# Kernel tuning notes

Hardware: AMD Instinct MI355X
Metric: run time of the kernel (lower is better)

## Reference

```python
import jax, jax.numpy as jnp
import numpy as np

N_NODES = 100000
N_EDGES = 3200000
IN_CH, HID, OUT_CH = 512, 16, 64


def gcn_conv(x, src, dst, W, b, n_nodes):
    """GCNConv: x @ W, then sym-normalized aggregation with self-loops."""
    xw = x @ W  # [N, F_out]
    loop = jnp.arange(n_nodes, dtype=src.dtype)
    s = jnp.concatenate([src, loop])  # sources (messages gathered here)
    d = jnp.concatenate([dst, loop])  # targets (messages scattered here)
    deg = jax.ops.segment_sum(jnp.ones_like(d, dtype=xw.dtype), d, num_segments=n_nodes)
    dinv = jnp.where(deg > 0, jax.lax.rsqrt(deg), 0.0)
    norm = dinv[s] * dinv[d]  # [E+N]
    msgs = xw[s] * norm[:, None]  # gather + scale
    out = jax.ops.segment_sum(msgs, d, num_segments=n_nodes)
    return out + b


def setup_inputs() -> dict:
    key = jax.random.key(0)
    k1, k2, k3, k4, k5 = jax.random.split(key, 5)
    x = jax.random.normal(k1, (N_NODES, IN_CH), dtype=jnp.float32)
    edge_index = jax.random.randint(k2, (2, N_EDGES), 0, N_NODES, dtype=jnp.int32)
    # Glorot-style init for GCNConv linear weights, zero bias (PyG default)
    W1 = jax.random.normal(k3, (IN_CH, HID), dtype=jnp.float32) * (1.0 / np.sqrt(IN_CH))
    b1 = jnp.zeros((HID,), dtype=jnp.float32)
    W2 = jax.random.normal(k4, (HID, OUT_CH), dtype=jnp.float32) * (1.0 / np.sqrt(HID))
    b2 = jnp.zeros((OUT_CH,), dtype=jnp.float32)
    return {"x": x, "edge_index": edge_index, "W1": W1, "b1": b1, "W2": W2, "b2": b2}


def reference(x, edge_index, W1, b1, W2, b2):
    # eval mode: dropout(p=0.5) is identity
    src, dst = edge_index[0], edge_index[1]
    h = gcn_conv(x, src, dst, W1, b1, N_NODES)
    h = jax.nn.relu(h)
    out = gcn_conv(h, src, dst, W2, b2, N_NODES)
    return out
```

## Files before the change

kernel.cpp:

```cpp
#include <hip/hip_runtime.h>

#define N_NODES 100000
#define N_EDGES 3200000
#define IN_CH 512
#define HID 16
#define OUT_CH 64

#define NB1 98
#define CAP1 34816
#define LEAF 64
#define CAP2 2560
#define NLEAF 1563
#define NLEAF_SLOTS (NB1 * 16)
#define BIN1_CHUNK 4096
#define BIN1_BLOCKS ((N_EDGES + BIN1_CHUNK - 1) / BIN1_CHUNK)
#define BIN2_SPLIT 9
#define BIN2_CHUNK 3872

typedef float f4 __attribute__((ext_vector_type(4)));
typedef unsigned int v2u __attribute__((ext_vector_type(2)));
typedef unsigned int v4u __attribute__((ext_vector_type(4)));

__device__ __forceinline__ unsigned rne(float f) {
    unsigned u = __float_as_uint(f);
    return (u + 0x7fffu + ((u >> 16) & 1u)) >> 16;
}
__device__ __forceinline__ v2u pk4(f4 f) {
    v2u r;
    r.x = rne(f.x) | (rne(f.y) << 16);
    r.y = rne(f.z) | (rne(f.w) << 16);
    return r;
}
__device__ __forceinline__ f4 up_lo(v4u v) {
    f4 r;
    r.x = __uint_as_float(v.x << 16);
    r.y = __uint_as_float(v.x & 0xffff0000u);
    r.z = __uint_as_float(v.y << 16);
    r.w = __uint_as_float(v.y & 0xffff0000u);
    return r;
}
__device__ __forceinline__ f4 up_hi(v4u v) {
    f4 r;
    r.x = __uint_as_float(v.z << 16);
    r.y = __uint_as_float(v.z & 0xffff0000u);
    r.z = __uint_as_float(v.w << 16);
    r.w = __uint_as_float(v.w & 0xffff0000u);
    return r;
}
__device__ __forceinline__ v4u pk8(f4 lo, f4 hi) {
    v4u r;
    r.x = rne(lo.x) | (rne(lo.y) << 16);
    r.y = rne(lo.z) | (rne(lo.w) << 16);
    r.z = rne(hi.x) | (rne(hi.y) << 16);
    r.w = rne(hi.z) | (rne(hi.w) << 16);
    return r;
}


__global__ void k_init_bcur(int* bcur1, int* bcur2, int* off) {
    int i = blockIdx.x * blockDim.x + threadIdx.x;
    if (i < NB1) bcur1[i] = i * CAP1;
    if (i < NLEAF_SLOTS) bcur2[i] = i * CAP2;
    if (i == 0) off[N_NODES] = N_EDGES;
}


__global__ __launch_bounds__(256) void k_bin1(const int* __restrict__ src,
                                              const int* __restrict__ dst,
                                              int* __restrict__ pairs1,
                                              int* __restrict__ bcur1) {
    __shared__ int cnt[NB1];
    __shared__ int base[NB1];
    const int tid = threadIdx.x;
    const int lo = blockIdx.x * BIN1_CHUNK;
    const int hi = min(lo + BIN1_CHUNK, N_EDGES);
    if (tid < NB1) cnt[tid] = 0;
    __syncthreads();
    for (int i = lo + tid; i < hi; i += 256) {
        int d = __builtin_nontemporal_load(dst + i);
        atomicAdd(&cnt[d >> 10], 1);
    }
    __syncthreads();
    if (tid < NB1 && cnt[tid] > 0) base[tid] = atomicAdd(&bcur1[tid], cnt[tid]);
    __syncthreads();
    if (tid < NB1) cnt[tid] = 0;
    __syncthreads();
    for (int i = lo + tid; i < hi; i += 256) {
        int d = __builtin_nontemporal_load(dst + i);
        int s = __builtin_nontemporal_load(src + i);
        int b = d >> 10;
        int r = atomicAdd(&cnt[b], 1);
        pairs1[base[b] + r] = (s << 10) | (d & 1023);
    }
}


__global__ __launch_bounds__(256) void k_bin2(const int* __restrict__ pairs1,
                                              const int* __restrict__ bcur1,
                                              int* __restrict__ pairs2,
                                              int* __restrict__ bcur2) {
    __shared__ int cnt[16];
    __shared__ int base[16];
    const int b = blockIdx.x / BIN2_SPLIT;
    const int s = blockIdx.x % BIN2_SPLIT;
    const int tid = threadIdx.x;
    const int len = bcur1[b] - b * CAP1;
    const int lo = b * CAP1 + min(s * BIN2_CHUNK, len);
    const int hi = b * CAP1 + min((s + 1) * BIN2_CHUNK, len);
    if (tid < 16) cnt[tid] = 0;
    __syncthreads();
    for (int i = lo + tid; i < hi; i += 256)
        atomicAdd(&cnt[(pairs1[i] & 1023) >> 6], 1);
    __syncthreads();
    if (tid < 16 && cnt[tid] > 0) base[tid] = atomicAdd(&bcur2[b * 16 + tid], cnt[tid]);
    __syncthreads();
    if (tid < 16) cnt[tid] = 0;
    __syncthreads();
    for (int i = lo + tid; i < hi; i += 256) {
        int e = pairs1[i];
        int l = (e & 1023) >> 6;
        int r = atomicAdd(&cnt[l], 1);
        pairs2[base[l] + r] = e;
    }
}


__global__ __launch_bounds__(256) void k_leafscan(const int* __restrict__ bcur2,
                                                  int* __restrict__ leafoff) {
    __shared__ int sm[256];
    __shared__ int carry;
    const int tid = threadIdx.x;
    if (tid == 0) carry = 0;
    __syncthreads();
    for (int r = 0; r < (NLEAF_SLOTS + 255) / 256; ++r) {
        int idx = r * 256 + tid;
        int v = (idx < NLEAF_SLOTS) ? (bcur2[idx] - idx * CAP2) : 0;
        sm[tid] = v;
        __syncthreads();
        for (int st = 1; st < 256; st <<= 1) {
            int t = (tid >= st) ? sm[tid - st] : 0;
            __syncthreads();
            sm[tid] += t;
            __syncthreads();
        }
        if (idx < NLEAF_SLOTS) leafoff[idx] = carry + sm[tid] - v;
        int tot = sm[255];
        __syncthreads();
        if (tid == 0) carry += tot;
        __syncthreads();
    }
}


__global__ __launch_bounds__(256) void k_scatter2(const int* __restrict__ pairs2,
                                                  const int* __restrict__ bcur2,
                                                  const int* __restrict__ leafoff,
                                                  int* __restrict__ off,
                                                  float* __restrict__ dinv,
                                                  int* __restrict__ csr) {
    __shared__ int cnt[LEAF];
    __shared__ int lcur[LEAF];
    __shared__ int buf[CAP2];
    const int leaf = blockIdx.x;
    const int tid = threadIdx.x;
    const int base2 = leaf * CAP2;
    const int len = min(bcur2[leaf] - base2, CAP2);
    const int obase = leafoff[leaf];
    if (tid < LEAF) cnt[tid] = 0;
    __syncthreads();
    for (int i = tid; i < len; i += 256)
        atomicAdd(&cnt[pairs2[base2 + i] & 63], 1);
    __syncthreads();
    if (tid < LEAF) {
        int v = cnt[tid];
        int s = v;
        for (int d = 1; d < LEAF; d <<= 1) {
            int t = __shfl_up(s, d, 64);
            if (tid >= d) s += t;
        }
        int excl = s - v;
        lcur[tid] = excl;
        int node = leaf * LEAF + tid;
        if (node < N_NODES) {
            off[node] = obase + excl;
            dinv[node] = rsqrtf((float)(1 + v));
        }
    }
    __syncthreads();
    for (int i = tid; i < len; i += 256) {
        int e = pairs2[base2 + i];
        int p = atomicAdd(&lcur[e & 63], 1);
        buf[p] = e >> 10;
    }
    __syncthreads();
    for (int i = tid; i < len; i += 256)
        csr[obase + i] = buf[i];
}


#define G1_BS 256
#define G1_NODES 128
#define G1_KT 64
#define G1_STRIDE (G1_KT + 4)

__global__ __launch_bounds__(G1_BS) void k_gemm1(const float* __restrict__ x,
                                                 const float* __restrict__ W1,
                                                 const float* __restrict__ dinv,
                                                 unsigned short* __restrict__ y1) {
    __shared__ float xt[G1_NODES * G1_STRIDE];
    __shared__ float wt[G1_KT * HID];
    const int tid = threadIdx.x;
    const int nl = tid >> 2;
    const int cg = tid & 3;
    const int node_base = blockIdx.x * G1_NODES;

    f4 acc0 = {0.f, 0.f, 0.f, 0.f};
    f4 acc1 = {0.f, 0.f, 0.f, 0.f};

    for (int kt = 0; kt < IN_CH; kt += G1_KT) {
        __syncthreads();
        for (int j = 0; j < 8; ++j) {
            int f = j * G1_BS + tid;
            int r = f >> 4;
            int c4 = f & 15;
            int gr = node_base + r;
            f4 v = {0.f, 0.f, 0.f, 0.f};
            if (gr < N_NODES)
                v = *(const f4*)(x + (size_t)gr * IN_CH + kt + c4 * 4);
            *(f4*)(xt + r * G1_STRIDE + c4 * 4) = v;
        }
        {
            int r = tid >> 2;
            int c4 = tid & 3;
            *(f4*)(wt + r * HID + c4 * 4) =
                *(const f4*)(W1 + (size_t)(kt + r) * HID + c4 * 4);
        }
        __syncthreads();

        for (int kk = 0; kk < G1_KT; kk += 4) {
            f4 x0 = *(const f4*)(xt + nl * G1_STRIDE + kk);
            f4 x1 = *(const f4*)(xt + (nl + 64) * G1_STRIDE + kk);
            f4 w0 = *(const f4*)(wt + (kk + 0) * HID + cg * 4);
            f4 w1 = *(const f4*)(wt + (kk + 1) * HID + cg * 4);
            f4 w2 = *(const f4*)(wt + (kk + 2) * HID + cg * 4);
            f4 w3 = *(const f4*)(wt + (kk + 3) * HID + cg * 4);
            acc0 += x0.x * w0; acc0 += x0.y * w1;
            acc0 += x0.z * w2; acc0 += x0.w * w3;
            acc1 += x1.x * w0; acc1 += x1.y * w1;
            acc1 += x1.z * w2; acc1 += x1.w * w3;
        }
    }

    int n0 = node_base + nl;
    int n1 = n0 + 64;
    if (n0 < N_NODES) {
        float dv = dinv[n0];
        __builtin_nontemporal_store(pk4(acc0 * dv),
            (v2u*)(y1 + (size_t)n0 * HID + cg * 4));
    }
    if (n1 < N_NODES) {
        float dv = dinv[n1];
        __builtin_nontemporal_store(pk4(acc1 * dv),
            (v2u*)(y1 + (size_t)n1 * HID + cg * 4));
    }
}


__global__ __launch_bounds__(256) void k_layer1(const unsigned short* __restrict__ y1,
                                                const int* __restrict__ off,
                                                const int* __restrict__ csr,
                                                const float* __restrict__ b1,
                                                unsigned short* __restrict__ y2) {
    int t = blockIdx.x * blockDim.x + threadIdx.x;
    int n = t >> 1;
    int hf = (t & 1) * 8;
    if (n >= N_NODES) return;
    int base = off[n];
    int cnt = off[n + 1] - base;
    f4 l0 = {0,0,0,0}, h0 = {0,0,0,0}, l1 = {0,0,0,0}, h1 = {0,0,0,0};
    f4 l2 = {0,0,0,0}, h2 = {0,0,0,0}, l3 = {0,0,0,0}, h3 = {0,0,0,0};
    int p = 0;
    for (; p + 4 <= cnt; p += 4) {
        int s0 = csr[base + p + 0];
        int s1 = csr[base + p + 1];
        int s2 = csr[base + p + 2];
        int s3 = csr[base + p + 3];
        v4u g0 = *(const v4u*)(y1 + (size_t)s0 * HID + hf);
        v4u g1 = *(const v4u*)(y1 + (size_t)s1 * HID + hf);
        v4u g2 = *(const v4u*)(y1 + (size_t)s2 * HID + hf);
        v4u g3 = *(const v4u*)(y1 + (size_t)s3 * HID + hf);
        l0 += up_lo(g0); h0 += up_hi(g0);
        l1 += up_lo(g1); h1 += up_hi(g1);
        l2 += up_lo(g2); h2 += up_hi(g2);
        l3 += up_lo(g3); h3 += up_hi(g3);
    }
    for (; p < cnt; ++p) {
        v4u g = *(const v4u*)(y1 + (size_t)csr[base + p] * HID + hf);
        l0 += up_lo(g); h0 += up_hi(g);
    }
    f4 alo = (l0 + l1) + (l2 + l3);
    f4 ahi = (h0 + h1) + (h2 + h3);
    float dv = rsqrtf((float)(cnt + 1));
    v4u gs = *(const v4u*)(y1 + (size_t)n * HID + hf);
    alo += up_lo(gs);
    ahi += up_hi(gs);
    f4 blo = ((const f4*)b1)[(t & 1) * 2 + 0];
    f4 bhi = ((const f4*)b1)[(t & 1) * 2 + 1];
    f4 rlo, rhi;
    rlo.x = fmaxf(dv * alo.x + blo.x, 0.f) * dv;
    rlo.y = fmaxf(dv * alo.y + blo.y, 0.f) * dv;
    rlo.z = fmaxf(dv * alo.z + blo.z, 0.f) * dv;
    rlo.w = fmaxf(dv * alo.w + blo.w, 0.f) * dv;
    rhi.x = fmaxf(dv * ahi.x + bhi.x, 0.f) * dv;
    rhi.y = fmaxf(dv * ahi.y + bhi.y, 0.f) * dv;
    rhi.z = fmaxf(dv * ahi.z + bhi.z, 0.f) * dv;
    rhi.w = fmaxf(dv * ahi.w + bhi.w, 0.f) * dv;
    __builtin_nontemporal_store(pk8(rlo, rhi), (v4u*)(y2 + (size_t)n * HID + hf));
}


__global__ __launch_bounds__(256) void k_layer2(const unsigned short* __restrict__ y2,
                                                const int* __restrict__ off,
                                                const int* __restrict__ csr,
                                                const float* __restrict__ W2,
                                                const float* __restrict__ b2,
                                                float* __restrict__ out) {
    __shared__ float w2[HID * OUT_CH];
    __shared__ float bs[OUT_CH];
    int tid = threadIdx.x;
    for (int j = tid; j < HID * OUT_CH; j += 256) w2[j] = W2[j];
    if (tid < OUT_CH) bs[tid] = b2[tid];
    __syncthreads();

    int t = blockIdx.x * blockDim.x + tid;
    int n = t >> 1;
    int cg = t & 1;
    int hf = cg * 8;
    if (n >= N_NODES) return;
    int base = off[n];
    int cnt = off[n + 1] - base;
    f4 l0 = {0,0,0,0}, h0 = {0,0,0,0}, l1 = {0,0,0,0}, h1 = {0,0,0,0};
    f4 l2 = {0,0,0,0}, h2 = {0,0,0,0}, l3 = {0,0,0,0}, h3 = {0,0,0,0};
    int p = 0;
    for (; p + 4 <= cnt; p += 4) {
        int s0 = csr[base + p + 0];
        int s1 = csr[base + p + 1];
        int s2 = csr[base + p + 2];
        int s3 = csr[base + p + 3];
        v4u g0 = *(const v4u*)(y2 + (size_t)s0 * HID + hf);
        v4u g1 = *(const v4u*)(y2 + (size_t)s1 * HID + hf);
        v4u g2 = *(const v4u*)(y2 + (size_t)s2 * HID + hf);
        v4u g3 = *(const v4u*)(y2 + (size_t)s3 * HID + hf);
        l0 += up_lo(g0); h0 += up_hi(g0);
        l1 += up_lo(g1); h1 += up_hi(g1);
        l2 += up_lo(g2); h2 += up_hi(g2);
        l3 += up_lo(g3); h3 += up_hi(g3);
    }
    for (; p < cnt; ++p) {
        v4u g = *(const v4u*)(y2 + (size_t)csr[base + p] * HID + hf);
        l0 += up_lo(g); h0 += up_hi(g);
    }
    f4 alo = (l0 + l1) + (l2 + l3);
    f4 ahi = (h0 + h1) + (h2 + h3);
    float dv = rsqrtf((float)(cnt + 1));
    v4u gs = *(const v4u*)(y2 + (size_t)n * HID + hf);
    alo += up_lo(gs);
    ahi += up_hi(gs);
    float zown[8] = {dv * alo.x, dv * alo.y, dv * alo.z, dv * alo.w,
                     dv * ahi.x, dv * ahi.y, dv * ahi.z, dv * ahi.w};
    float z[16];
#pragma unroll
    for (int j = 0; j < 8; ++j) {
        float zp = __shfl_xor(zown[j], 1, 64);
        z[hf + j] = zown[j];
        z[(8 - hf) + j] = zp;
    }
    f4 o[8];
#pragma unroll
    for (int j = 0; j < 8; ++j) o[j] = ((const f4*)bs)[j * 2 + cg];
#pragma unroll
    for (int cc = 0; cc < HID; ++cc) {
        const float* wr = w2 + cc * OUT_CH;
        float zz = z[cc];
#pragma unroll
        for (int j = 0; j < 8; ++j)
            o[j] += zz * *(const f4*)(wr + (j * 2 + cg) * 4);
    }
    float* orow = out + (size_t)n * OUT_CH;
#pragma unroll
    for (int j = 0; j < 8; ++j)
        __builtin_nontemporal_store(o[j], (f4*)(orow + (j * 2 + cg) * 4));
}


extern "C" void kernel_launch(void* const* d_in, const int* in_sizes, int n_in,
                              void* d_out, int out_size, void* d_ws, size_t ws_size,
                              hipStream_t stream) {
    const float* x  = (const float*)d_in[0];
    const int*   ei = (const int*)d_in[1];
    const float* W1 = (const float*)d_in[2];
    const float* b1 = (const float*)d_in[3];
    const float* W2 = (const float*)d_in[4];
    const float* b2 = (const float*)d_in[5];
    float* out = (float*)d_out;

    const int* src = ei;
    const int* dst = ei + N_EDGES;

    char* w = (char*)d_ws;
    const size_t SN = 409600;
    float* dinv     = (float*)(w);
    int*   off      = (int*)(w + SN);
    int*   bcur1    = (int*)(w + 2 * SN);
    int*   bcur2    = (int*)(w + 2 * SN + 8192);
    int*   leafoff  = (int*)(w + 2 * SN + 16384);
    char*  regB     = w + 3 * SN;
    int*   pairs1   = (int*)regB;
    int*   csr      = (int*)regB;
    char*  regC     = regB + (size_t)NB1 * CAP1 * 4;
    int*   pairs2   = (int*)regC;
    unsigned short* y1 = (unsigned short*)regC;
    unsigned short* y2 = (unsigned short*)(regC + 3200000);

    k_init_bcur<<<(NLEAF_SLOTS + 255) / 256, 256, 0, stream>>>(bcur1, bcur2, off);
    k_bin1<<<BIN1_BLOCKS, 256, 0, stream>>>(src, dst, pairs1, bcur1);
    k_bin2<<<NB1 * BIN2_SPLIT, 256, 0, stream>>>(pairs1, bcur1, pairs2, bcur2);
    k_leafscan<<<1, 256, 0, stream>>>(bcur2, leafoff);
    k_scatter2<<<NLEAF, 256, 0, stream>>>(pairs2, bcur2, leafoff, off, dinv, csr);
    k_gemm1<<<(N_NODES + G1_NODES - 1) / G1_NODES, G1_BS, 0, stream>>>(x, W1, dinv, y1);
    k_layer1<<<(N_NODES * 2 + 255) / 256, 256, 0, stream>>>(y1, off, csr, b1, y2);
    k_layer2<<<(N_NODES * 2 + 255) / 256, 256, 0, stream>>>(y2, off, csr, W2, b2, out);
}
```

Before: 214.2 us.

## Replace two-level edge binning with single-pass 256-node buckets and block-local CSR scatter

Result: slower. 224.6 us (+4.8%).

```diff
diff --git a/kernel.cpp b/kernel.cpp
--- a/kernel.cpp
+++ b/kernel.cpp
@@ -6,16 +6,10 @@
 #define HID 16
 #define OUT_CH 64
 
-#define NB1 98
-#define CAP1 34816
-#define LEAF 64
-#define CAP2 2560
-#define NLEAF 1563
-#define NLEAF_SLOTS (NB1 * 16)
+#define NB 391
+#define BCAP 9472
 #define BIN1_CHUNK 4096
 #define BIN1_BLOCKS ((N_EDGES + BIN1_CHUNK - 1) / BIN1_CHUNK)
-#define BIN2_SPLIT 9
-#define BIN2_CHUNK 3872
 
 typedef float f4 __attribute__((ext_vector_type(4)));
 typedef unsigned int v2u __attribute__((ext_vector_type(2)));
@@ -57,10 +51,9 @@
 }
 
 
-__global__ void k_init_bcur(int* bcur1, int* bcur2, int* off) {
+__global__ void k_init(int* bcur1, int* off) {
     int i = blockIdx.x * blockDim.x + threadIdx.x;
-    if (i < NB1) bcur1[i] = i * CAP1;
-    if (i < NLEAF_SLOTS) bcur2[i] = i * CAP2;
+    if (i < NB) bcur1[i] = i * BCAP;
     if (i == 0) off[N_NODES] = N_EDGES;
 }
 
@@ -69,132 +62,95 @@
                                               const int* __restrict__ dst,
                                               int* __restrict__ pairs1,
                                               int* __restrict__ bcur1) {
-    __shared__ int cnt[NB1];
-    __shared__ int base[NB1];
+    __shared__ int cnt[NB];
+    __shared__ int base[NB];
     const int tid = threadIdx.x;
     const int lo = blockIdx.x * BIN1_CHUNK;
     const int hi = min(lo + BIN1_CHUNK, N_EDGES);
-    if (tid < NB1) cnt[tid] = 0;
+    for (int j = tid; j < NB; j += 256) cnt[j] = 0;
     __syncthreads();
     for (int i = lo + tid; i < hi; i += 256) {
         int d = __builtin_nontemporal_load(dst + i);
-        atomicAdd(&cnt[d >> 10], 1);
-    }
-    __syncthreads();
-    if (tid < NB1 && cnt[tid] > 0) base[tid] = atomicAdd(&bcur1[tid], cnt[tid]);
-    __syncthreads();
-    if (tid < NB1) cnt[tid] = 0;
+        atomicAdd(&cnt[d >> 8], 1);
+    }
+    __syncthreads();
+    for (int j = tid; j < NB; j += 256)
+        if (cnt[j] > 0) base[j] = atomicAdd(&bcur1[j], cnt[j]);
+    __syncthreads();
+    for (int j = tid; j < NB; j += 256) cnt[j] = 0;
     __syncthreads();
     for (int i = lo + tid; i < hi; i += 256) {
         int d = __builtin_nontemporal_load(dst + i);
         int s = __builtin_nontemporal_load(src + i);
-        int b = d >> 10;
+        int b = d >> 8;
         int r = atomicAdd(&cnt[b], 1);
-        pairs1[base[b] + r] = (s << 10) | (d & 1023);
-    }
-}
-
-
-__global__ __launch_bounds__(256) void k_bin2(const int* __restrict__ pairs1,
-                                              const int* __restrict__ bcur1,
-                                              int* __restrict__ pairs2,
-                                              int* __restrict__ bcur2) {
-    __shared__ int cnt[16];
-    __shared__ int base[16];
-    const int b = blockIdx.x / BIN2_SPLIT;
-    const int s = blockIdx.x % BIN2_SPLIT;
+        pairs1[base[b] + r] = (s << 8) | (d & 255);
+    }
+}
+
+
+__global__ __launch_bounds__(512) void k_bucketscan(const int* __restrict__ bcur1,
+                                                    int* __restrict__ bucketoff) {
+    __shared__ int sm[512];
     const int tid = threadIdx.x;
-    const int len = bcur1[b] - b * CAP1;
-    const int lo = b * CAP1 + min(s * BIN2_CHUNK, len);
-    const int hi = b * CAP1 + min((s + 1) * BIN2_CHUNK, len);
-    if (tid < 16) cnt[tid] = 0;
-    __syncthreads();
-    for (int i = lo + tid; i < hi; i += 256)
-        atomicAdd(&cnt[(pairs1[i] & 1023) >> 6], 1);
-    __syncthreads();
-    if (tid < 16 && cnt[tid] > 0) base[tid] = atomicAdd(&bcur2[b * 16 + tid], cnt[tid]);
-    __syncthreads();
-    if (tid < 16) cnt[tid] = 0;
-    __syncthreads();
-    for (int i = lo + tid; i < hi; i += 256) {
-        int e = pairs1[i];
-        int l = (e & 1023) >> 6;
-        int r = atomicAdd(&cnt[l], 1);
-        pairs2[base[l] + r] = e;
-    }
-}
-
-
-__global__ __launch_bounds__(256) void k_leafscan(const int* __restrict__ bcur2,
-                                                  int* __restrict__ leafoff) {
-    __shared__ int sm[256];
-    __shared__ int carry;
+    int v = (tid < NB) ? (bcur1[tid] - tid * BCAP) : 0;
+    sm[tid] = v;
+    __syncthreads();
+    for (int st = 1; st < 512; st <<= 1) {
+        int t = (tid >= st) ? sm[tid - st] : 0;
+        __syncthreads();
+        sm[tid] += t;
+        __syncthreads();
+    }
+    if (tid < NB) bucketoff[tid] = sm[tid] - v;
+}
+
+
+__global__ __launch_bounds__(256) void k_scatterXL(const int* __restrict__ pairs1,
+                                                   const int* __restrict__ bcur1,
+                                                   const int* __restrict__ bucketoff,
+                                                   int* __restrict__ off,
+                                                   float* __restrict__ dinv,
+                                                   int* __restrict__ csr) {
+    __shared__ int cnt[256];
+    __shared__ int lcur[256];
+    __shared__ int buf[BCAP];
+    const int b = blockIdx.x;
     const int tid = threadIdx.x;
-    if (tid == 0) carry = 0;
-    __syncthreads();
-    for (int r = 0; r < (NLEAF_SLOTS + 255) / 256; ++r) {
-        int idx = r * 256 + tid;
-        int v = (idx < NLEAF_SLOTS) ? (bcur2[idx] - idx * CAP2) : 0;
-        sm[tid] = v;
-        __syncthreads();
-        for (int st = 1; st < 256; st <<= 1) {
-            int t = (tid >= st) ? sm[tid - st] : 0;
-            __syncthreads();
-            sm[tid] += t;
-            __syncthreads();
-        }
-        if (idx < NLEAF_SLOTS) leafoff[idx] = carry + sm[tid] - v;
-        int tot = sm[255];
-        __syncthreads();
-        if (tid == 0) carry += tot;
-        __syncthreads();
-    }
-}
-
-
-__global__ __launch_bounds__(256) void k_scatter2(const int* __restrict__ pairs2,
-                                                  const int* __restrict__ bcur2,
-                                                  const int* __restrict__ leafoff,
-                                                  int* __restrict__ off,
-                                                  float* __restrict__ dinv,
-                                                  int* __restrict__ csr) {
-    __shared__ int cnt[LEAF];
-    __shared__ int lcur[LEAF];
-    __shared__ int buf[CAP2];
-    const int leaf = blockIdx.x;
-    const int tid = threadIdx.x;
-    const int base2 = leaf * CAP2;
-    const int len = min(bcur2[leaf] - base2, CAP2);
-    const int obase = leafoff[leaf];
-    if (tid < LEAF) cnt[tid] = 0;
+    const int base1 = b * BCAP;
+    const int len = min(bcur1[b] - base1, BCAP);
+    const int gbase = bucketoff[b];
+    cnt[tid] = 0;
     __syncthreads();
     for (int i = tid; i < len; i += 256)
-        atomicAdd(&cnt[pairs2[base2 + i] & 63], 1);
-    __syncthreads();
-    if (tid < LEAF) {
-        int v = cnt[tid];
-        int s = v;
-        for (int d = 1; d < LEAF; d <<= 1) {
-            int t = __shfl_up(s, d, 64);
-            if (tid >= d) s += t;
-        }
-        int excl = s - v;
-        lcur[tid] = excl;
-        int node = leaf * LEAF + tid;
-        if (node < N_NODES) {
-            off[node] = obase + excl;
-            dinv[node] = rsqrtf((float)(1 + v));
-        }
+        atomicAdd(&cnt[pairs1[base1 + i] & 255], 1);
+    __syncthreads();
+    int v = cnt[tid];
+    lcur[tid] = v;
+    __syncthreads();
+    for (int st = 1; st < 256; st <<= 1) {
+        int t = (tid >= st) ? lcur[tid - st] : 0;
+        __syncthreads();
+        lcur[tid] += t;
+        __syncthreads();
+    }
+    int excl = lcur[tid] - v;
+    __syncthreads();
+    lcur[tid] = excl;
+    int node = b * 256 + tid;
+    if (node < N_NODES) {
+        off[node] = gbase + excl;
+        dinv[node] = rsqrtf((float)(1 + v));
     }
     __syncthreads();
     for (int i = tid; i < len; i += 256) {
-        int e = pairs2[base2 + i];
-        int p = atomicAdd(&lcur[e & 63], 1);
-        buf[p] = e >> 10;
+        int e = pairs1[base1 + i];
+        int p = atomicAdd(&lcur[e & 255], 1);
+        buf[p] = e >> 8;
     }
     __syncthreads();
     for (int i = tid; i < len; i += 256)
-        csr[obase + i] = buf[i];
+        csr[gbase + i] = buf[i];
 }
 
 
@@ -409,24 +365,21 @@
 
     char* w = (char*)d_ws;
     const size_t SN = 409600;
-    float* dinv     = (float*)(w);
-    int*   off      = (int*)(w + SN);
-    int*   bcur1    = (int*)(w + 2 * SN);
-    int*   bcur2    = (int*)(w + 2 * SN + 8192);
-    int*   leafoff  = (int*)(w + 2 * SN + 16384);
-    char*  regB     = w + 3 * SN;
-    int*   pairs1   = (int*)regB;
-    int*   csr      = (int*)regB;
-    char*  regC     = regB + (size_t)NB1 * CAP1 * 4;
-    int*   pairs2   = (int*)regC;
+    float* dinv      = (float*)(w);
+    int*   off       = (int*)(w + SN);
+    int*   bcur1     = (int*)(w + 2 * SN);
+    int*   bucketoff = (int*)(w + 2 * SN + 8192);
+    char*  regB      = w + 3 * SN;
+    int*   pairs1    = (int*)regB;
+    int*   csr       = (int*)(regB + (size_t)NB * BCAP * 4);
+    char*  regC      = regB + (size_t)NB * BCAP * 4 + 12800000;
     unsigned short* y1 = (unsigned short*)regC;
     unsigned short* y2 = (unsigned short*)(regC + 3200000);
 
-    k_init_bcur<<<(NLEAF_SLOTS + 255) / 256, 256, 0, stream>>>(bcur1, bcur2, off);
+    k_init<<<(NB + 255) / 256, 256, 0, stream>>>(bcur1, off);
     k_bin1<<<BIN1_BLOCKS, 256, 0, stream>>>(src, dst, pairs1, bcur1);
-    k_bin2<<<NB1 * BIN2_SPLIT, 256, 0, stream>>>(pairs1, bcur1, pairs2, bcur2);
-    k_leafscan<<<1, 256, 0, stream>>>(bcur2, leafoff);
-    k_scatter2<<<NLEAF, 256, 0, stream>>>(pairs2, bcur2, leafoff, off, dinv, csr);
+    k_bucketscan<<<1, 512, 0, stream>>>(bcur1, bucketoff);
+    k_scatterXL<<<NB, 256, 0, stream>>>(pairs1, bcur1, bucketoff, off, dinv, csr);
     k_gemm1<<<(N_NODES + G1_NODES - 1) / G1_NODES, G1_BS, 0, stream>>>(x, W1, dinv, y1);
     k_layer1<<<(N_NODES * 2 + 255) / 256, 256, 0, stream>>>(y1, off, csr, b1, y2);
     k_layer2<<<(N_NODES * 2 + 255) / 256, 256, 0, stream>>>(y2, off, csr, W2, b2, out);
```
